# Optimization experiments

Hardware: AMD Instinct MI355X
Metric: run time of the kernel (lower is better)

The kernel has to match this reference:

```python
import jax, jax.numpy as jnp
import numpy as np

INTRA_W, TYPE_W, INTER_W = 1.0, 0.5, 0.5
MARGIN, TAU, EPS = 1.0, 0.1, 1e-8
N, D = 200000, 256          # nodes, feature dim
NT, EPT = 4, 2048           # n types, edges per type
E = NT * EPT                # 8192 hyperedges
SAMP_PER_TYPE = 100         # max_edges_per_type for intra loss
MAX_PAIRS = 500             # inter-loss pair sample


def setup_inputs() -> dict:
    key = jax.random.key(0)
    k1, k2, k3, k4, k5 = jax.random.split(key, 5)
    z_nodes = jax.random.normal(k1, (N, D), dtype=jnp.float32)
    # deterministic variable edge sizes in [8, 56]
    sizes = 8 + (np.arange(E) * 7919) % 49
    M = int(sizes.sum())  # 262128
    member_edge_id = jnp.asarray(np.repeat(np.arange(E), sizes), dtype=jnp.int32)
    member_node_idx = jax.random.randint(k2, (M,), 0, N, dtype=jnp.int32)
    edge_type = jnp.asarray(np.repeat(np.arange(NT), EPT), dtype=jnp.int32)
    # intra-loss edge sampling: 100 edges per type (mimics torch.randperm sampling)
    perm = jax.random.permutation(k3, EPT)
    intra_sample = jnp.concatenate(
        [perm[:SAMP_PER_TYPE] + t * EPT for t in range(NT)]).astype(jnp.int32)
    # inter-loss pair sampling (mimics torch.randint + self-collision fixup)
    pair_idx1 = jax.random.randint(k4, (MAX_PAIRS,), 0, E, dtype=jnp.int32)
    pair_idx2 = jax.random.randint(k5, (MAX_PAIRS,), 0, E, dtype=jnp.int32)
    pair_idx2 = jnp.where(pair_idx1 == pair_idx2, (pair_idx2 + 1) % E, pair_idx2)
    return dict(z_nodes=z_nodes, member_node_idx=member_node_idx,
                member_edge_id=member_edge_id, edge_type=edge_type,
                intra_sample=intra_sample, pair_idx1=pair_idx1, pair_idx2=pair_idx2)


def reference(z_nodes, member_node_idx, member_edge_id, edge_type,
              intra_sample, pair_idx1, pair_idx2):
    # --- ragged segment mean: hyperedge embeddings ---
    gathered = z_nodes[member_node_idx]                               # [M, D]
    counts = jax.ops.segment_sum(jnp.ones_like(member_edge_id, jnp.float32),
                                 member_edge_id, num_segments=E)      # [E]
    edge_sum = jax.ops.segment_sum(gathered, member_edge_id, num_segments=E)
    edge_emb = edge_sum / counts[:, None]                             # [E, D]

    # --- B1: intra-hyperedge loss over sampled edges ---
    sq_dist = jnp.sum((gathered - edge_emb[member_edge_id]) ** 2, axis=-1)  # [M]
    per_edge = jax.ops.segment_sum(sq_dist, member_edge_id, num_segments=E) / counts
    intra = jnp.mean(per_edge[intra_sample])

    # --- B2: type contrastive InfoNCE ---
    z = edge_emb / jnp.linalg.norm(edge_emb, axis=-1, keepdims=True)  # [E, D]
    sim = jnp.matmul(z, z.T) / TAU                                    # [E, E]
    self_mask = jnp.eye(E, dtype=bool)
    exp_sim = jnp.exp(sim) * (~self_mask)
    denom = exp_sim.sum(axis=1)
    type_mask = (edge_type[None, :] == edge_type[:, None]) & ~self_mask
    numer = jnp.sum(exp_sim * type_mask, axis=1)
    per_row = -jnp.log((numer + EPS) / (denom + EPS))
    has_pos = type_mask.sum(axis=1) > 0
    type_loss = jnp.sum(jnp.where(has_pos, per_row, 0.0)) / jnp.maximum(
        has_pos.sum().astype(per_row.dtype), 1.0)

    # --- B3: inter-hyperedge margin loss on sampled pairs ---
    dist = jnp.linalg.norm(edge_emb[pair_idx1] - edge_emb[pair_idx2], axis=-1)
    inter = jnp.mean(jax.nn.relu(MARGIN - dist) ** 2)

    total = INTRA_W * intra + TYPE_W * type_loss + INTER_W * inter
    return jnp.stack([intra, type_loss, inter, total])
```

## Files before the change

kernel.cpp:

```cpp
#include <hip/hip_runtime.h>


#define DDIM 256
#define NTYPES 4
#define TAU_INV 10.0f
#define EPSV 1e-8f

#define COLSEG 512
#define CTILE 64
#define NT2 (COLSEG / CTILE)

typedef short v8s __attribute__((ext_vector_type(8)));
typedef float v4f __attribute__((ext_vector_type(4)));
typedef unsigned short ushort_t;

__device__ __forceinline__ int lower_bound_i(const int* __restrict__ a, int n, int key) {
  int lo = 0, hi = n;
  while (lo < hi) { int mid = (lo + hi) >> 1; if (a[mid] < key) lo = mid + 1; else hi = mid; }
  return lo;
}

__device__ __forceinline__ ushort_t f2bf(float f) {
  union { float f; unsigned u; } v; v.f = f;
  unsigned r = v.u + 0x7FFFu + ((v.u >> 16) & 1u);
  return (ushort_t)(r >> 16);
}

__device__ __forceinline__ float bf2f(ushort_t u) {
  union { unsigned u; float f; } v; v.u = ((unsigned)u) << 16;
  return v.f;
}

__device__ __forceinline__ void load_lds16(const ushort_t* g, ushort_t* l) {
  __builtin_amdgcn_global_load_lds(
      (const __attribute__((address_space(1))) unsigned int*)g,
      (__attribute__((address_space(3))) unsigned int*)l, 16, 0, 0);
}

__global__ __launch_bounds__(256)
void boundary_kernel(const int* __restrict__ mei, int M, int E,
                     int* __restrict__ off, float* __restrict__ typeSums,
                     float* __restrict__ scalars) {
  int i = blockIdx.x * 256 + threadIdx.x;
  if (i < M - 1) {
    int a = mei[i], b = mei[i + 1];
    for (int e = a + 1; e <= b; ++e) off[e] = i + 1;
  }
  if (i == 0) { off[0] = 0; off[E] = M; }
  if (i < E * NTYPES) typeSums[i] = 0.f;
  if (i < 8) scalars[i] = 0.f;
}

__global__ __launch_bounds__(256)
void edge_kernel(const float* __restrict__ z, const int* __restrict__ mni,
                 const int* __restrict__ off, int M, int E,
                 ushort_t* __restrict__ zn, float* __restrict__ emb,
                 float* __restrict__ per_edge, float* __restrict__ selfArr) {
  __shared__ int shIdx[64];
  __shared__ float shAcc[1024];
  __shared__ float shRed[12];
  int e = blockIdx.x;
  int tid = threadIdx.x;

  int s = off[e];
  int t = off[e + 1];
  int cnt = t - s;
  if (tid < cnt) shIdx[tid] = mni[s + tid];
  __syncthreads();

  int group = tid >> 6, lane = tid & 63;
  float4 acc = make_float4(0.f, 0.f, 0.f, 0.f);
  float sq = 0.f;
  int m = group;
  for (; m + 12 < cnt; m += 16) {
    int n0 = shIdx[m], n1 = shIdx[m + 4], n2 = shIdx[m + 8], n3 = shIdx[m + 12];
    float4 v0 = *(const float4*)(z + (size_t)n0 * DDIM + lane * 4);
    float4 v1 = *(const float4*)(z + (size_t)n1 * DDIM + lane * 4);
    float4 v2 = *(const float4*)(z + (size_t)n2 * DDIM + lane * 4);
    float4 v3 = *(const float4*)(z + (size_t)n3 * DDIM + lane * 4);
    acc.x += v0.x; acc.y += v0.y; acc.z += v0.z; acc.w += v0.w;
    sq += v0.x * v0.x + v0.y * v0.y + v0.z * v0.z + v0.w * v0.w;
    acc.x += v1.x; acc.y += v1.y; acc.z += v1.z; acc.w += v1.w;
    sq += v1.x * v1.x + v1.y * v1.y + v1.z * v1.z + v1.w * v1.w;
    acc.x += v2.x; acc.y += v2.y; acc.z += v2.z; acc.w += v2.w;
    sq += v2.x * v2.x + v2.y * v2.y + v2.z * v2.z + v2.w * v2.w;
    acc.x += v3.x; acc.y += v3.y; acc.z += v3.z; acc.w += v3.w;
    sq += v3.x * v3.x + v3.y * v3.y + v3.z * v3.z + v3.w * v3.w;
  }
  for (; m < cnt; m += 4) {
    int n0 = shIdx[m];
    float4 v0 = *(const float4*)(z + (size_t)n0 * DDIM + lane * 4);
    acc.x += v0.x; acc.y += v0.y; acc.z += v0.z; acc.w += v0.w;
    sq += v0.x * v0.x + v0.y * v0.y + v0.z * v0.z + v0.w * v0.w;
  }

  *(float4*)(&shAcc[tid * 4]) = acc;
  __syncthreads();
  int d = tid;
  float total = shAcc[d] + shAcc[256 + d] + shAcc[512 + d] + shAcc[768 + d];
  float inv = 1.0f / (float)cnt;
  float mu = total * inv;
  emb[(size_t)e * DDIM + d] = mu;

  float a1 = sq, a2 = mu * mu;
  #pragma unroll
  for (int off2 = 32; off2 > 0; off2 >>= 1) {
    a1 += __shfl_down(a1, off2);
    a2 += __shfl_down(a2, off2);
  }
  if (lane == 0) { shRed[group] = a1; shRed[4 + group] = a2; }
  __syncthreads();
  if (tid == 0) {
    float sqT = shRed[0] + shRed[1] + shRed[2] + shRed[3];
    float musqT = shRed[4] + shRed[5] + shRed[6] + shRed[7];
    per_edge[e] = sqT * inv - musqT;
    shRed[8] = musqT;
  }
  __syncthreads();
  float rn = rsqrtf(shRed[8]);
  ushort_t znv = f2bf(mu * rn);
  zn[(size_t)e * DDIM + d] = znv;

  float zq = bf2f(znv);
  float a3 = zq * zq;
  #pragma unroll
  for (int off2 = 32; off2 > 0; off2 >>= 1) a3 += __shfl_down(a3, off2);
  if (lane == 0) shRed[group] = a3;
  __syncthreads();
  if (tid == 0)
    selfArr[e] = __expf(TAU_INV * (shRed[0] + shRed[1] + shRed[2] + shRed[3]));
}

__global__ __launch_bounds__(256)
void gemm_kernel(const ushort_t* __restrict__ zn, const int* __restrict__ edge_type,
                 int E, float* __restrict__ typeSums) {
  __shared__ __align__(16) ushort_t sB[CTILE * DDIM];

  int tid = threadIdx.x;
  int lane = tid & 63, wave = tid >> 6;
  int quad = lane >> 4, l15 = lane & 15;
  int rb = blockIdx.y;
  int cs = blockIdx.x;
  int row0 = rb * 256 + wave * 64;
  int c0 = cs * COLSEG;
  int T = edge_type[c0];

  v8s aF[4][8];
  #pragma unroll
  for (int rt = 0; rt < 4; ++rt) {
    const ushort_t* base = zn + (size_t)(row0 + rt * 16 + l15) * DDIM + quad * 8;
    #pragma unroll
    for (int ks = 0; ks < 8; ++ks)
      aF[rt][ks] = *(const v8s*)(base + ks * 32);
  }

  float acc[4][4] = {};

  for (int t = 0; t < NT2; ++t) {
    const ushort_t* src = zn + (size_t)(c0 + t * CTILE) * DDIM;
    #pragma unroll
    for (int it = 0; it < 8; ++it) {
      int f = it * 256 + tid;
      load_lds16(src + f * 8, &sB[f * 8]);
    }
    __syncthreads();

    #pragma unroll
    for (int h = 0; h < 2; ++h) {
      v4f c[4][2];
      #pragma unroll
      for (int rt = 0; rt < 4; ++rt)
        #pragma unroll
        for (int ct = 0; ct < 2; ++ct)
          c[rt][ct] = (v4f){0.f, 0.f, 0.f, 0.f};

      #pragma unroll
      for (int ks = 0; ks < 8; ++ks) {
        #pragma unroll
        for (int ct = 0; ct < 2; ++ct) {
          v8s b = *(const v8s*)(&sB[((h * 2 + ct) * 16 + l15) * DDIM + ks * 32 + quad * 8]);
          #pragma unroll
          for (int rt = 0; rt < 4; ++rt)
            c[rt][ct] = __builtin_amdgcn_mfma_f32_16x16x32_bf16(aF[rt][ks], b, c[rt][ct], 0, 0, 0);
        }
      }
      #pragma unroll
      for (int rt = 0; rt < 4; ++rt)
        #pragma unroll
        for (int ct = 0; ct < 2; ++ct)
          #pragma unroll
          for (int rr = 0; rr < 4; ++rr)
            acc[rt][rr] += __expf(c[rt][ct][rr] * TAU_INV);
    }
    __syncthreads();
  }

  #pragma unroll
  for (int rt = 0; rt < 4; ++rt) {
    #pragma unroll
    for (int rr = 0; rr < 4; ++rr) {
      float v = acc[rt][rr];
      v += __shfl_xor(v, 1);
      v += __shfl_xor(v, 2);
      v += __shfl_xor(v, 4);
      v += __shfl_xor(v, 8);
      if (l15 == 0) {
        int row = row0 + rt * 16 + quad * 4 + rr;
        atomicAdd(&typeSums[row * NTYPES + T], v);
      }
    }
  }
}

__global__ __launch_bounds__(256)
void tail_kernel(const float* __restrict__ emb, const float* __restrict__ per_edge,
                 const int* __restrict__ intra_sample, int nIntra,
                 const int* __restrict__ p1, const int* __restrict__ p2, int nPairs,
                 const float* __restrict__ typeSums, const float* __restrict__ selfArr,
                 const int* __restrict__ edge_type, int E, float* __restrict__ scalars) {
  __shared__ float sh[8];
  int b = blockIdx.x;
  int tid = threadIdx.x;
  int lane = tid & 63, wave = tid >> 6;
  int nRowBlocks = E / 256;

  if (b < nRowBlocks) {
    int row = b * 256 + tid;
    int t = edge_type[row];
    float self = selfArr[row];
    float s0 = typeSums[row * 4 + 0];
    float s1 = typeSums[row * 4 + 1];
    float s2 = typeSums[row * 4 + 2];
    float s3 = typeSums[row * 4 + 3];
    float denom = (s0 + s1 + s2 + s3) - self;
    float own = (t == 0) ? s0 : (t == 1) ? s1 : (t == 2) ? s2 : s3;
    float numer = own - self;
    float pr = 0.f, hp = 0.f;
    int cs = lower_bound_i(edge_type, E, t);
    int ce = lower_bound_i(edge_type, E, t + 1);
    if (ce - cs - 1 > 0) {
      hp = 1.f;
      pr = -__logf((numer + EPSV) / (denom + EPSV));
    }
    float a1 = pr, a2 = hp;
    #pragma unroll
    for (int off = 32; off > 0; off >>= 1) {
      a1 += __shfl_down(a1, off);
      a2 += __shfl_down(a2, off);
    }
    if (lane == 0) { sh[wave] = a1; sh[4 + wave] = a2; }
    __syncthreads();
    if (tid == 0) {
      atomicAdd(&scalars[2], sh[0] + sh[1] + sh[2] + sh[3]);
      atomicAdd(&scalars[3], sh[4] + sh[5] + sh[6] + sh[7]);
    }
  } else if (b == nRowBlocks) {
    float s = 0.f;
    for (int i = tid; i < nIntra; i += 256) s += per_edge[intra_sample[i]];
    #pragma unroll
    for (int off = 32; off > 0; off >>= 1) s += __shfl_down(s, off);
    if (lane == 0) sh[wave] = s;
    __syncthreads();
    if (tid == 0) atomicAdd(&scalars[0], sh[0] + sh[1] + sh[2] + sh[3]);
  } else {
    int p = (b - nRowBlocks - 1) * 4 + wave;
    if (p < nPairs) {
      int i1 = p1[p], i2 = p2[p];
      const float4* r1 = (const float4*)(emb + (size_t)i1 * DDIM);
      const float4* r2 = (const float4*)(emb + (size_t)i2 * DDIM);
      float4 x = r1[lane], y = r2[lane];
      float d0 = x.x - y.x, d1 = x.y - y.y, d2 = x.z - y.z, d3 = x.w - y.w;
      float s = d0 * d0 + d1 * d1 + d2 * d2 + d3 * d3;
      #pragma unroll
      for (int off = 32; off > 0; off >>= 1) s += __shfl_down(s, off);
      if (lane == 0) {
        float dist = sqrtf(s);
        float v = fmaxf(1.0f - dist, 0.0f);
        atomicAdd(&scalars[1], v * v);
      }
    }
  }
}

__global__ void finalize_kernel(const float* __restrict__ scalars, int nIntra, int nPairs,
                                float* __restrict__ out) {
  if (threadIdx.x == 0) {
    float intra = scalars[0] / (float)nIntra;
    float inter = scalars[1] / (float)nPairs;
    float typeL = scalars[2] / fmaxf(scalars[3], 1.f);
    out[0] = intra;
    out[1] = typeL;
    out[2] = inter;
    out[3] = 1.0f * intra + 0.5f * typeL + 0.5f * inter;
  }
}

extern "C" void kernel_launch(void* const* d_in, const int* in_sizes, int n_in,
                              void* d_out, int out_size, void* d_ws, size_t ws_size,
                              hipStream_t stream) {
  const float* z      = (const float*)d_in[0];
  const int* mni      = (const int*)d_in[1];
  const int* mei      = (const int*)d_in[2];
  const int* etype    = (const int*)d_in[3];
  const int* intra_s  = (const int*)d_in[4];
  const int* p1       = (const int*)d_in[5];
  const int* p2       = (const int*)d_in[6];
  int M      = in_sizes[1];
  int E      = in_sizes[3];
  int nIntra = in_sizes[4];
  int nPairs = in_sizes[5];

  char* ws = (char*)d_ws;
  ushort_t* zn    = (ushort_t*)ws;
  float* emb      = (float*)(ws + (size_t)E * DDIM * 2);
  float* per_edge = (float*)(ws + (size_t)E * DDIM * 6);
  float* typeSums = per_edge + E;
  float* selfArr  = typeSums + (size_t)E * NTYPES;
  float* scalars  = selfArr + E;
  int* off        = (int*)(scalars + 8);

  float* out = (float*)d_out;

  boundary_kernel<<<(M + 254) / 256, 256, 0, stream>>>(mei, M, E, off, typeSums, scalars);

  edge_kernel<<<E, 256, 0, stream>>>(z, mni, off, M, E, zn, emb, per_edge, selfArr);

  dim3 g(E / COLSEG, E / 256);
  gemm_kernel<<<g, 256, 0, stream>>>(zn, etype, E, typeSums);

  int nPB = (nPairs + 3) / 4;
  tail_kernel<<<E / 256 + 1 + nPB, 256, 0, stream>>>(
      emb, per_edge, intra_s, nIntra, p1, p2, nPairs,
      typeSums, selfArr, etype, E, scalars);

  finalize_kernel<<<1, 64, 0, stream>>>(scalars, nIntra, nPairs, out);
}
```

Baseline: 348.6 us.

## Map one hyperedge per wave in edge kernel, removing LDS and block syncs

The edge aggregation kernel now gives each hyperedge a single 64-lane wave, with four edges per block, instead of a whole 256-thread block. All reductions use wave shuffles, so the shared-memory staging, cross-group sum and __syncthreads barriers are gone, and each wave issues 8 independent gather loads per iteration. Each wave now walks every member serially, so a wave's latency grows with edge size. Member indices are read straight from global memory rather than staged in LDS.

```diff
diff --git a/kernel.cpp b/kernel.cpp
--- a/kernel.cpp
+++ b/kernel.cpp
@@ -56,28 +56,28 @@
                  const int* __restrict__ off, int M, int E,
                  ushort_t* __restrict__ zn, float* __restrict__ emb,
                  float* __restrict__ per_edge, float* __restrict__ selfArr) {
-  __shared__ int shIdx[64];
-  __shared__ float shAcc[1024];
-  __shared__ float shRed[12];
-  int e = blockIdx.x;
-  int tid = threadIdx.x;
-
-  int s = off[e];
-  int t = off[e + 1];
+  int wave = threadIdx.x >> 6, lane = threadIdx.x & 63;
+  int e = blockIdx.x * 4 + wave;
+  int s = off[e], t = off[e + 1];
   int cnt = t - s;
-  if (tid < cnt) shIdx[tid] = mni[s + tid];
-  __syncthreads();
-
-  int group = tid >> 6, lane = tid & 63;
+  const float* zl = z + (size_t)lane * 4;
+
   float4 acc = make_float4(0.f, 0.f, 0.f, 0.f);
   float sq = 0.f;
-  int m = group;
-  for (; m + 12 < cnt; m += 16) {
-    int n0 = shIdx[m], n1 = shIdx[m + 4], n2 = shIdx[m + 8], n3 = shIdx[m + 12];
-    float4 v0 = *(const float4*)(z + (size_t)n0 * DDIM + lane * 4);
-    float4 v1 = *(const float4*)(z + (size_t)n1 * DDIM + lane * 4);
-    float4 v2 = *(const float4*)(z + (size_t)n2 * DDIM + lane * 4);
-    float4 v3 = *(const float4*)(z + (size_t)n3 * DDIM + lane * 4);
+  int m = 0;
+  for (; m + 8 <= cnt; m += 8) {
+    int n0 = mni[s + m + 0], n1 = mni[s + m + 1];
+    int n2 = mni[s + m + 2], n3 = mni[s + m + 3];
+    int n4 = mni[s + m + 4], n5 = mni[s + m + 5];
+    int n6 = mni[s + m + 6], n7 = mni[s + m + 7];
+    float4 v0 = *(const float4*)(zl + (size_t)n0 * DDIM);
+    float4 v1 = *(const float4*)(zl + (size_t)n1 * DDIM);
+    float4 v2 = *(const float4*)(zl + (size_t)n2 * DDIM);
+    float4 v3 = *(const float4*)(zl + (size_t)n3 * DDIM);
+    float4 v4 = *(const float4*)(zl + (size_t)n4 * DDIM);
+    float4 v5 = *(const float4*)(zl + (size_t)n5 * DDIM);
+    float4 v6 = *(const float4*)(zl + (size_t)n6 * DDIM);
+    float4 v7 = *(const float4*)(zl + (size_t)n7 * DDIM);
     acc.x += v0.x; acc.y += v0.y; acc.z += v0.z; acc.w += v0.w;
     sq += v0.x * v0.x + v0.y * v0.y + v0.z * v0.z + v0.w * v0.w;
     acc.x += v1.x; acc.y += v1.y; acc.z += v1.z; acc.w += v1.w;
@@ -86,49 +86,45 @@
     sq += v2.x * v2.x + v2.y * v2.y + v2.z * v2.z + v2.w * v2.w;
     acc.x += v3.x; acc.y += v3.y; acc.z += v3.z; acc.w += v3.w;
     sq += v3.x * v3.x + v3.y * v3.y + v3.z * v3.z + v3.w * v3.w;
-  }
-  for (; m < cnt; m += 4) {
-    int n0 = shIdx[m];
-    float4 v0 = *(const float4*)(z + (size_t)n0 * DDIM + lane * 4);
+    acc.x += v4.x; acc.y += v4.y; acc.z += v4.z; acc.w += v4.w;
+    sq += v4.x * v4.x + v4.y * v4.y + v4.z * v4.z + v4.w * v4.w;
+    acc.x += v5.x; acc.y += v5.y; acc.z += v5.z; acc.w += v5.w;
+    sq += v5.x * v5.x + v5.y * v5.y + v5.z * v5.z + v5.w * v5.w;
+    acc.x += v6.x; acc.y += v6.y; acc.z += v6.z; acc.w += v6.w;
+    sq += v6.x * v6.x + v6.y * v6.y + v6.z * v6.z + v6.w * v6.w;
+    acc.x += v7.x; acc.y += v7.y; acc.z += v7.z; acc.w += v7.w;
+    sq += v7.x * v7.x + v7.y * v7.y + v7.z * v7.z + v7.w * v7.w;
+  }
+  for (; m < cnt; ++m) {
+    int n0 = mni[s + m];
+    float4 v0 = *(const float4*)(zl + (size_t)n0 * DDIM);
     acc.x += v0.x; acc.y += v0.y; acc.z += v0.z; acc.w += v0.w;
     sq += v0.x * v0.x + v0.y * v0.y + v0.z * v0.z + v0.w * v0.w;
   }
 
-  *(float4*)(&shAcc[tid * 4]) = acc;
-  __syncthreads();
-  int d = tid;
-  float total = shAcc[d] + shAcc[256 + d] + shAcc[512 + d] + shAcc[768 + d];
   float inv = 1.0f / (float)cnt;
-  float mu = total * inv;
-  emb[(size_t)e * DDIM + d] = mu;
-
-  float a1 = sq, a2 = mu * mu;
+  float4 mu = make_float4(acc.x * inv, acc.y * inv, acc.z * inv, acc.w * inv);
+  *(float4*)(emb + (size_t)e * DDIM + lane * 4) = mu;
+
+  float musq = mu.x * mu.x + mu.y * mu.y + mu.z * mu.z + mu.w * mu.w;
   #pragma unroll
-  for (int off2 = 32; off2 > 0; off2 >>= 1) {
-    a1 += __shfl_down(a1, off2);
-    a2 += __shfl_down(a2, off2);
-  }
-  if (lane == 0) { shRed[group] = a1; shRed[4 + group] = a2; }
-  __syncthreads();
-  if (tid == 0) {
-    float sqT = shRed[0] + shRed[1] + shRed[2] + shRed[3];
-    float musqT = shRed[4] + shRed[5] + shRed[6] + shRed[7];
-    per_edge[e] = sqT * inv - musqT;
-    shRed[8] = musqT;
-  }
-  __syncthreads();
-  float rn = rsqrtf(shRed[8]);
-  ushort_t znv = f2bf(mu * rn);
-  zn[(size_t)e * DDIM + d] = znv;
-
-  float zq = bf2f(znv);
-  float a3 = zq * zq;
+  for (int o = 1; o < 64; o <<= 1) {
+    sq += __shfl_xor(sq, o);
+    musq += __shfl_xor(musq, o);
+  }
+  if (lane == 0) per_edge[e] = sq * inv - musq;
+
+  float rn = rsqrtf(musq);
+  ushort_t q0 = f2bf(mu.x * rn), q1 = f2bf(mu.y * rn);
+  ushort_t q2 = f2bf(mu.z * rn), q3 = f2bf(mu.w * rn);
+  ushort4 pack = make_ushort4(q0, q1, q2, q3);
+  *(ushort4*)(zn + (size_t)e * DDIM + lane * 4) = pack;
+
+  float z0 = bf2f(q0), z1 = bf2f(q1), z2 = bf2f(q2), z3 = bf2f(q3);
+  float sf = z0 * z0 + z1 * z1 + z2 * z2 + z3 * z3;
   #pragma unroll
-  for (int off2 = 32; off2 > 0; off2 >>= 1) a3 += __shfl_down(a3, off2);
-  if (lane == 0) shRed[group] = a3;
-  __syncthreads();
-  if (tid == 0)
-    selfArr[e] = __expf(TAU_INV * (shRed[0] + shRed[1] + shRed[2] + shRed[3]));
+  for (int o = 1; o < 64; o <<= 1) sf += __shfl_xor(sf, o);
+  if (lane == 0) selfArr[e] = __expf(TAU_INV * sf);
 }
 
 __global__ __launch_bounds__(256)
@@ -323,7 +319,7 @@
 
   boundary_kernel<<<(M + 254) / 256, 256, 0, stream>>>(mei, M, E, off, typeSums, scalars);
 
-  edge_kernel<<<E, 256, 0, stream>>>(z, mni, off, M, E, zn, emb, per_edge, selfArr);
+  edge_kernel<<<E / 4, 256, 0, stream>>>(z, mni, off, M, E, zn, emb, per_edge, selfArr);
 
   dim3 g(E / COLSEG, E / 256);
   gemm_kernel<<<g, 256, 0, stream>>>(zn, etype, E, typeSums);
```

After: 352.6 us. About the same (+1.2%).
